# Kernel optimization log

Hardware: AMD Instinct MI355X
Metric: run time of the kernel (lower is better)

The kernel has to match this reference:

```python
import jax, jax.numpy as jnp
import numpy as np

TIME_SEG_LEN = 5
PRED_STEPS = 1
B, N, D = 4, 4096, 4
F1, F2 = 32, 64  # cnn filters; F2 must equal GCSConv/Dense width 64


def _conv1d_time(x, Wc1, bc1, Wc2, bc2):
    # x: [B, N, T, D] -> per-node temporal CNN collapsing T=5 -> 1 -> [B, N, F2]
    b, n, t, d = x.shape
    xr = x.reshape(b * n, t, d)
    dn = ('NWC', 'WIO', 'NWC')
    h = jax.lax.conv_general_dilated(xr, Wc1, (1,), 'VALID', dimension_numbers=dn) + bc1
    h = jax.nn.relu(h)
    h = jax.lax.conv_general_dilated(h, Wc2, (1,), 'VALID', dimension_numbers=dn) + bc2
    return h.reshape(b, n, -1)  # [B, N, F2]


def setup_inputs() -> dict:
    key = jax.random.key(0)
    ks = jax.random.split(key, 12)
    time_segs = jax.random.normal(ks[0], (B, TIME_SEG_LEN, N, D), dtype=jnp.float32)
    edges = jax.random.randint(ks[1], (N, N), 0, 2, dtype=jnp.int32)
    s = lambda *sh: 1.0 / np.sqrt(sh[-2] if len(sh) > 1 else sh[0])
    return {
        'time_segs': time_segs,
        'edges': edges,
        'Wc1': jax.random.normal(ks[2], (3, D, F1), dtype=jnp.float32) * 0.3,
        'bc1': jnp.zeros((F1,), jnp.float32),
        'Wc2': jax.random.normal(ks[3], (3, F1, F2), dtype=jnp.float32) * 0.1,
        'bc2': jnp.zeros((F2,), jnp.float32),
        'Wg1': jax.random.normal(ks[4], (F2, 64), dtype=jnp.float32) * 0.125,
        'bg': jnp.zeros((64,), jnp.float32),
        'Wd': jax.random.normal(ks[5], (F2 + 64, 64), dtype=jnp.float32) * 0.09,
        'bd': jnp.zeros((64,), jnp.float32),
        'Wo': jax.random.normal(ks[6], (64, D), dtype=jnp.float32) * 0.125,
        'bo': jnp.zeros((D,), jnp.float32),
    }


def reference(time_segs, edges, Wc1, bc1, Wc2, bc2, Wg1, bg, Wd, bd, Wo, bo):
    A = edges.astype(jnp.float32)
    n = A.shape[0]
    deg = jnp.sum(A, axis=-1, keepdims=True)              # row degree
    A_norm = A / jnp.where(deg > 0, deg, 1.0)             # D^-1 A (symmetric=False)
    A_nd = A_norm * (1.0 - jnp.eye(n, dtype=A.dtype))     # self-edge masking of X row j == zeroing diag
    col_deg = jnp.sum(A, axis=0)                          # e = np.sum(edges, axis=0)
    alive = (col_deg != 0).astype(time_segs.dtype)[None, :, None]  # zero-degree nodes -> zeros branch

    ext = jnp.transpose(time_segs, (0, 2, 1, 3))          # [B, N, T, D]
    for i in range(PRED_STEPS):
        seg = ext[:, :, i:, :]                            # [B, N, 5, D]
        cond = _conv1d_time(seg, Wc1, bc1, Wc2, bc2)      # [B, N, F2]
        # Vectorized per-node masked GCSConv: row j of tanh(A X_j W1 + X_j W2 + b)
        # with X_j = X zeroed at node j. Skip term vanishes at row j.
        agg = jnp.einsum('jk,bkf->bjf', A_nd, cond)       # [B, N, F2]
        G = jnp.tanh(agg @ Wg1 + bg) * alive              # [B, N, 64]
        h = jax.nn.relu(jnp.concatenate([cond, G], axis=-1) @ Wd + bd)
        nxt = seg[:, :, -1, :] + jnp.tanh(h @ Wo + bo)    # residual update [B, N, D]
        ext = jnp.concatenate([ext, nxt[:, :, None, :]], axis=2)
    out = jnp.transpose(ext, (0, 2, 1, 3))                # [B, T+P, N, D]
    return out[:, TIME_SEG_LEN:, :, :]                    # [B, pred_steps, N, D]
```

## Files before the change

kernel.cpp:

```cpp
#include <hip/hip_runtime.h>
#include <math.h>

typedef unsigned short ushort_t;
typedef unsigned int uint_t;
typedef unsigned long long u64_t;
typedef __attribute__((ext_vector_type(8))) __bf16 bf16x8;
typedef __attribute__((ext_vector_type(4))) float f32x4;

#define NN 4096
#define TT 5
#define F1 32
#define F2 64

__device__ __forceinline__ ushort_t f2bf(float x) {
    union { float f; uint_t u; } v; v.f = x;
    uint_t r = (v.u + 0x7FFFu + ((v.u >> 16) & 1u)) >> 16;
    return (ushort_t)r;
}
__device__ __forceinline__ float bf16f(float x) {
    union { float f; uint_t u; } v; v.f = x;
    v.u = (v.u + 0x7FFFu + ((v.u >> 16) & 1u)) & 0xFFFF0000u;
    return v.f;
}
__device__ __forceinline__ uint_t pk2(float a, float b) {
    return (uint_t)f2bf(a) | ((uint_t)f2bf(b) << 16);
}
__device__ __forceinline__ float tanh_fast(float x) {
    const float xc = fminf(fmaxf(x, -10.f), 10.f);
    const float e = __expf(2.f * xc);
    return (e - 1.f) * __builtin_amdgcn_rcpf(e + 1.f);
}

#define H1S 104
#define CBS 80
__global__ __launch_bounds__(256) void k1_cond(
    const float* __restrict__ ts, const float* __restrict__ Wc1, const float* __restrict__ bc1,
    const float* __restrict__ Wc2, const float* __restrict__ bc2,
    float* __restrict__ condf, ushort_t* __restrict__ condT)
{
    const int b = blockIdx.y;
    const int j0 = blockIdx.x * 64;
    const int t = threadIdx.x;

    __shared__ float sWc1[384];
    __shared__ float sbc1[F1];
    __shared__ float sbc2[F2];
    __shared__ ushort_t sWc2T[64 * H1S];
    __shared__ ushort_t h1B[64 * H1S];
    __shared__ ushort_t scb[64 * CBS];

    for (int i = t; i < 384; i += 256) sWc1[i] = Wc1[i];
    if (t < F1) sbc1[t] = bc1[t];
    if (t < F2) sbc2[t] = bc2[t];
    for (int i = t; i < 96 * 64; i += 256) {
        const int e = i >> 6, f = i & 63;
        sWc2T[f * H1S + e] = f2bf(Wc2[i]);
    }
    __syncthreads();

    {
        const int n = t & 63, f10 = (t >> 6) * 8;
        const int j = j0 + n;
        float4 x[5];
        #pragma unroll
        for (int tt = 0; tt < 5; ++tt)
            x[tt] = *(const float4*)(ts + ((((size_t)b * TT + tt) << 12) + j) * 4);
        #pragma unroll
        for (int tt0 = 0; tt0 < 3; ++tt0) {
            #pragma unroll
            for (int ff = 0; ff < 8; ++ff) {
                const int f1 = f10 + ff;
                float a = sbc1[f1];
                #pragma unroll
                for (int dt = 0; dt < 3; ++dt) {
                    const float4 xx = x[tt0 + dt];
                    a += xx.x * sWc1[(dt * 4 + 0) * F1 + f1];
                    a += xx.y * sWc1[(dt * 4 + 1) * F1 + f1];
                    a += xx.z * sWc1[(dt * 4 + 2) * F1 + f1];
                    a += xx.w * sWc1[(dt * 4 + 3) * F1 + f1];
                }
                h1B[n * H1S + tt0 * 32 + f1] = f2bf(fmaxf(a, 0.f));
            }
        }
    }
    __syncthreads();

    {
        const int w = t >> 6, l = t & 63;
        const int m0 = w * 16, kseg = (l >> 4) * 8;
        f32x4 acc[4] = {};
        #pragma unroll
        for (int ks = 0; ks < 3; ++ks) {
            const bf16x8 av = *(const bf16x8*)&h1B[(m0 + (l & 15)) * H1S + ks * 32 + kseg];
            #pragma unroll
            for (int ct = 0; ct < 4; ++ct) {
                const bf16x8 bv = *(const bf16x8*)&sWc2T[(ct * 16 + (l & 15)) * H1S + ks * 32 + kseg];
                acc[ct] = __builtin_amdgcn_mfma_f32_16x16x32_bf16(av, bv, acc[ct], 0, 0, 0);
            }
        }
        #pragma unroll
        for (int ct = 0; ct < 4; ++ct)
            #pragma unroll
            for (int i = 0; i < 4; ++i) {
                const int row = m0 + (l >> 4) * 4 + i;
                const int col = ct * 16 + (l & 15);
                const float c = acc[ct][i] + sbc2[col];
                condf[((((size_t)b << 12) + j0 + row) << 6) + col] = c;
                scb[col * CBS + row] = f2bf(c);
            }
    }
    __syncthreads();
    {
        const int f2 = t >> 2, seg = t & 3;
        ushort_t* dst = condT + (((size_t)b * 64 + f2) << 12) + j0 + seg * 16;
        *(uint4*)dst = *(const uint4*)&scb[f2 * CBS + seg * 16];
        *(uint4*)(dst + 8) = *(const uint4*)&scb[f2 * CBS + seg * 16 + 8];
    }
}

__device__ __forceinline__ void stage_chunk(
    const int4 pa, int it, int kq, ushort_t* dstbuf, int soff, uint_t& regm, int& cnt)
{
    const u64_t b0 = __ballot(pa.x != 0);
    const u64_t b1 = __ballot(pa.y != 0);
    const u64_t b2 = __ballot(pa.z != 0);
    const u64_t b3 = __ballot(pa.w != 0);
    const uint_t m0 = (uint_t)(b0 | (b0 >> 32)), m1 = (uint_t)(b1 | (b1 >> 32));
    const uint_t m2 = (uint_t)(b2 | (b2 >> 32)), m3 = (uint_t)(b3 | (b3 >> 32));
    const uint_t nib = ((m0 >> kq) & 1u) | (((m1 >> kq) & 1u) << 1) |
                       (((m2 >> kq) & 1u) << 2) | (((m3 >> kq) & 1u) << 3);
    regm |= nib << (it * 4);
    cnt += (pa.x != 0) + (pa.y != 0) + (pa.z != 0) + (pa.w != 0);
    const uint_t h01 = (pa.x ? 0x3F80u : 0u) | (pa.y ? 0x3F800000u : 0u);
    const uint_t h23 = (pa.z ? 0x3F80u : 0u) | (pa.w ? 0x3F800000u : 0u);
    *(uint2*)(dstbuf + soff) = make_uint2(h01, h23);
}

__global__ __launch_bounds__(1024, 8) void k3_gemm(
    const int* __restrict__ edges, const ushort_t* __restrict__ condT,
    float* __restrict__ agg0, float* __restrict__ agg1,
    float* __restrict__ agg2, float* __restrict__ agg3,
    int* __restrict__ degI, uint_t* __restrict__ colbits)
{
    const int t = threadIdx.x;
    const int stripe = blockIdx.x >> 2, ks4 = blockIdx.x & 3;
    const int j0 = stripe * 32, kb = ks4 * 1024;

    __shared__ __align__(16) ushort_t abuf[8][4096];

    const int w = t >> 6, l = t & 63;
    const int r = t >> 5, kq = t & 31;
    const int rl = r & 15, rh = r >> 4;
    const int ks_s = kq >> 3, q_s = (kq >> 1) & 3;
    const int soff = (rh * 2048 + ks_s * 512 + (q_s * 16 + rl) * 8 + (kq & 1) * 4) ^ (q_s << 4);
    const int aoff = (l * 8) ^ ((l >> 4) << 4);

    const int* ep = edges + (size_t)(j0 + r) * NN + kb + kq * 4;
    const ushort_t* bp = condT + (size_t)(w * 16 + (l & 15)) * NN + kb + (l >> 4) * 8;

    uint_t regm = 0; int cnt = 0;
    int4 pa[4];

    #pragma unroll
    for (int c = 0; c < 4; ++c) pa[c] = *(const int4*)(ep + c * 128);
    #pragma unroll
    for (int c = 0; c < 4; ++c) stage_chunk(pa[c], c, kq, &abuf[c][0], soff, regm, cnt);
    __syncthreads();

    #pragma unroll
    for (int c = 0; c < 4; ++c) pa[c] = *(const int4*)(ep + (c + 4) * 128);

    f32x4 acc0 = {0.f, 0.f, 0.f, 0.f};
    f32x4 acc1 = {0.f, 0.f, 0.f, 0.f};

    #pragma unroll
    for (int ch = 0; ch < 4; ++ch) {
        const ushort_t* ab = &abuf[ch][0];
        const ushort_t* bpi = bp + ch * 128;
        #pragma unroll
        for (int ks = 0; ks < 4; ++ks) {
            const bf16x8 bfv = *(const bf16x8*)(bpi + ks * 32);
            const bf16x8 a0 = *(const bf16x8*)(ab + ks * 512 + aoff);
            const bf16x8 a1 = *(const bf16x8*)(ab + 2048 + ks * 512 + aoff);
            acc0 = __builtin_amdgcn_mfma_f32_16x16x32_bf16(a0, bfv, acc0, 0, 0, 0);
            acc1 = __builtin_amdgcn_mfma_f32_16x16x32_bf16(a1, bfv, acc1, 0, 0, 0);
        }
    }
    #pragma unroll
    for (int c = 0; c < 4; ++c) stage_chunk(pa[c], c + 4, kq, &abuf[c + 4][0], soff, regm, cnt);
    __syncthreads();

    #pragma unroll
    for (int ch = 4; ch < 8; ++ch) {
        const ushort_t* ab = &abuf[ch][0];
        const ushort_t* bpi = bp + ch * 128;
        #pragma unroll
        for (int ks = 0; ks < 4; ++ks) {
            const bf16x8 bfv = *(const bf16x8*)(bpi + ks * 32);
            const bf16x8 a0 = *(const bf16x8*)(ab + ks * 512 + aoff);
            const bf16x8 a1 = *(const bf16x8*)(ab + 2048 + ks * 512 + aoff);
            acc0 = __builtin_amdgcn_mfma_f32_16x16x32_bf16(a0, bfv, acc0, 0, 0, 0);
            acc1 = __builtin_amdgcn_mfma_f32_16x16x32_bf16(a1, bfv, acc1, 0, 0, 0);
        }
    }

    {
        float* aggS = (ks4 == 0) ? agg0 : (ks4 == 1) ? agg1 : (ks4 == 2) ? agg2 : agg3;
        const int col = w * 16 + (l & 15);
        float* dst = aggS + ((size_t)(col >> 6) * NN << 6) + (col & 63);
        #pragma unroll
        for (int i = 0; i < 4; ++i) {
            const int ja = j0 + (l >> 4) * 4 + i;
            dst[(size_t)ja << 6] = acc0[i];
            dst[(size_t)(ja + 16) << 6] = acc1[i];
        }
    }
    {
        int s = cnt;
        #pragma unroll
        for (int off = 16; off >= 1; off >>= 1) s += __shfl_down(s, off, 32);
        if (kq == 0) atomicAdd(&degI[j0 + r], s);
    }
    __syncthreads();
    uint_t* colsh = (uint_t*)&abuf[0][0];
    if (l < 32) colsh[w * 32 + kq] = regm;
    __syncthreads();
    if (t < 32) {
        uint_t v = 0;
        #pragma unroll
        for (int w2 = 0; w2 < 16; ++w2) v |= colsh[w2 * 32 + t];
        colsh[512 + t] = v;
    }
    __syncthreads();
    if (t < 32) {
        const int it = t >> 2, koct = t & 3;
        uint_t word = 0;
        #pragma unroll
        for (int s2 = 0; s2 < 8; ++s2)
            word |= ((colsh[512 + koct * 8 + s2] >> (it * 4)) & 15u) << (s2 * 4);
        atomicOr(&colbits[(kb >> 5) + t], word);
    }
}

#define WGS 88
#define WDS 136
#define HS  69
__global__ __launch_bounds__(256) void k4_mlp(
    const float* __restrict__ ts, const int* __restrict__ edges,
    const float* __restrict__ condf,
    const float* __restrict__ agg0, const float* __restrict__ agg1,
    const float* __restrict__ agg2, const float* __restrict__ agg3,
    const int* __restrict__ degI, const uint_t* __restrict__ colbits,
    const float* __restrict__ Wg1, const float* __restrict__ bg,
    const float* __restrict__ Wd, const float* __restrict__ bd,
    const float* __restrict__ Wo, const float* __restrict__ bo,
    float* __restrict__ out)
{
    const int b = blockIdx.y;
    const int j0 = blockIdx.x * 64;
    const int t = threadIdx.x;

    __shared__ ushort_t sWg1T[64 * WGS];
    __shared__ ushort_t sWdT[64 * WDS];
    __shared__ ushort_t aggB[64 * WGS];
    __shared__ ushort_t catB[64 * WDS];
    __shared__ float sH[64 * HS];
    __shared__ float sWo[256];
    __shared__ float sbg[64], sbd[64], sbo[4], sAlive[64];

    for (int i = t; i < 4096; i += 256) {
        const int in = i >> 6, o = i & 63;
        sWg1T[o * WGS + in] = f2bf(Wg1[i]);
    }
    for (int i = t; i < 8192; i += 256) {
        const int in = i >> 6, o = i & 63;
        sWdT[o * WDS + in] = f2bf(Wd[i]);
    }
    if (t < 256) sWo[t] = Wo[t];
    if (t < 64) { sbg[t] = bg[t]; sbd[t] = bd[t]; }
    if (t < 4) sbo[t] = bo[t];
    if (t < 64) {
        const int j = j0 + t;
        sAlive[t] = (float)((colbits[j >> 5] >> (j & 31)) & 1u);
    }
    {
        const int r = t >> 2, fs = t & 3;
        const int j = j0 + r;
        const float dv = (float)degI[j];
        const float inv = 1.f / (dv > 0.f ? dv : 1.f);
        const float dgf = edges[(size_t)j * NN + j] ? 1.f : 0.f;
        const size_t base = (((size_t)b << 12) + j) << 6;
        #pragma unroll
        for (int q = 0; q < 4; ++q) {
            const int f = fs * 16 + q * 4;
            const float4 a0 = *(const float4*)(agg0 + base + f);
            const float4 a1 = *(const float4*)(agg1 + base + f);
            const float4 a2 = *(const float4*)(agg2 + base + f);
            const float4 a3 = *(const float4*)(agg3 + base + f);
            const float4 c4 = *(const float4*)(condf + base + f);
            const float n0 = (a0.x + a1.x + a2.x + a3.x - dgf * bf16f(c4.x)) * inv;
            const float n1 = (a0.y + a1.y + a2.y + a3.y - dgf * bf16f(c4.y)) * inv;
            const float n2 = (a0.z + a1.z + a2.z + a3.z - dgf * bf16f(c4.z)) * inv;
            const float n3 = (a0.w + a1.w + a2.w + a3.w - dgf * bf16f(c4.w)) * inv;
            *(uint2*)&aggB[r * WGS + f] = make_uint2(pk2(n0, n1), pk2(n2, n3));
            *(uint2*)&catB[r * WDS + f] = make_uint2(pk2(c4.x, c4.y), pk2(c4.z, c4.w));
        }
    }
    __syncthreads();

    const int w = t >> 6, l = t & 63;
    const int m0 = w * 16, kseg = (l >> 4) * 8;

    {
        f32x4 acc[4] = {};
        #pragma unroll
        for (int ks = 0; ks < 2; ++ks) {
            const bf16x8 av = *(const bf16x8*)&aggB[(m0 + (l & 15)) * WGS + ks * 32 + kseg];
            #pragma unroll
            for (int ct = 0; ct < 4; ++ct) {
                const bf16x8 bv = *(const bf16x8*)&sWg1T[(ct * 16 + (l & 15)) * WGS + ks * 32 + kseg];
                acc[ct] = __builtin_amdgcn_mfma_f32_16x16x32_bf16(av, bv, acc[ct], 0, 0, 0);
            }
        }
        #pragma unroll
        for (int ct = 0; ct < 4; ++ct)
            #pragma unroll
            for (int i = 0; i < 4; ++i) {
                const int row = m0 + (l >> 4) * 4 + i;
                const int col = ct * 16 + (l & 15);
                const float g = tanh_fast(acc[ct][i] + sbg[col]) * sAlive[row];
                catB[row * WDS + 64 + col] = f2bf(g);
            }
    }
    __syncthreads();
    {
        f32x4 acc[4] = {};
        #pragma unroll
        for (int ks = 0; ks < 4; ++ks) {
            const bf16x8 av = *(const bf16x8*)&catB[(m0 + (l & 15)) * WDS + ks * 32 + kseg];
            #pragma unroll
            for (int ct = 0; ct < 4; ++ct) {
                const bf16x8 bv = *(const bf16x8*)&sWdT[(ct * 16 + (l & 15)) * WDS + ks * 32 + kseg];
                acc[ct] = __builtin_amdgcn_mfma_f32_16x16x32_bf16(av, bv, acc[ct], 0, 0, 0);
            }
        }
        #pragma unroll
        for (int ct = 0; ct < 4; ++ct)
            #pragma unroll
            for (int i = 0; i < 4; ++i) {
                const int row = m0 + (l >> 4) * 4 + i;
                const int col = ct * 16 + (l & 15);
                sH[row * HS + col] = fmaxf(acc[ct][i] + sbd[col], 0.f);
            }
    }
    __syncthreads();
    {
        const int r = t >> 2, d = t & 3;
        const int j = j0 + r;
        float s = sbo[d];
        #pragma unroll 8
        for (int f = 0; f < 64; ++f) s += sH[r * HS + f] * sWo[f * 4 + d];
        const float segl = ts[((((size_t)b * TT + 4) << 12) + j) * 4 + d];
        out[((((size_t)b << 12) + j) << 2) + d] = segl + tanh_fast(s);
    }
}

extern "C" void kernel_launch(void* const* d_in, const int* in_sizes, int n_in,
                              void* d_out, int out_size, void* d_ws, size_t ws_size,
                              hipStream_t stream)
{
    (void)in_sizes; (void)n_in; (void)out_size; (void)ws_size;
    const float* ts    = (const float*)d_in[0];
    const int*   edges = (const int*)d_in[1];
    const float* Wc1   = (const float*)d_in[2];
    const float* bc1   = (const float*)d_in[3];
    const float* Wc2   = (const float*)d_in[4];
    const float* bc2   = (const float*)d_in[5];
    const float* Wg1   = (const float*)d_in[6];
    const float* bg    = (const float*)d_in[7];
    const float* Wd    = (const float*)d_in[8];
    const float* bd    = (const float*)d_in[9];
    const float* Wo    = (const float*)d_in[10];
    const float* bo    = (const float*)d_in[11];
    float* out = (float*)d_out;

    char* ws = (char*)d_ws;
    ushort_t* condT   = (ushort_t*)(ws);
    float*    condf   = (float*)(ws + (size_t)(2 << 20));
    float*    agg0    = (float*)(ws + (size_t)(6 << 20));
    float*    agg1    = (float*)(ws + (size_t)(10 << 20));
    float*    agg2    = (float*)(ws + (size_t)(14 << 20));
    float*    agg3    = (float*)(ws + (size_t)(18 << 20));
    int*      degI    = (int*)(ws + (size_t)(22 << 20));
    uint_t*   colbits = (uint_t*)(ws + (size_t)(22 << 20) + 16384);

    hipMemsetAsync(degI, 0, 16384 + 512, stream);

    k1_cond<<<dim3(64, 4), 256, 0, stream>>>(ts, Wc1, bc1, Wc2, bc2, condf, condT);
    k3_gemm<<<512, 1024, 0, stream>>>(edges, condT, agg0, agg1, agg2, agg3, degI, colbits);
    k4_mlp<<<dim3(64, 4), 256, 0, stream>>>(ts, edges, condf, agg0, agg1, agg2, agg3,
                                            degI, colbits, Wg1, bg, Wd, bd, Wo, bo, out);
}
```

Before: 166.1 us.

## Pack adjacency into bitmask in a separate kernel and feed GEMM from bits

Adds a k2_bits kernel that streams the int32 edge matrix once, packs it into a 1-bit-per-edge mask, and computes row degrees. The GEMM kernel then reads the compact bitmask instead of the 64 MB int matrix and expands it to bf16 in shared memory in a single stage, with simplified column-alive bookkeeping through a shared atomicOr. The edge matrix is still read in full once, so the total bytes read barely change. The change adds a kernel launch and a serial dependency, and it loses the earlier overlap of edge loads with MFMA work.

```diff
diff --git a/kernel.cpp b/kernel.cpp
--- a/kernel.cpp
+++ b/kernel.cpp
@@ -118,63 +118,68 @@
     }
 }
 
-__device__ __forceinline__ void stage_chunk(
-    const int4 pa, int it, int kq, ushort_t* dstbuf, int soff, uint_t& regm, int& cnt)
-{
-    const u64_t b0 = __ballot(pa.x != 0);
-    const u64_t b1 = __ballot(pa.y != 0);
-    const u64_t b2 = __ballot(pa.z != 0);
-    const u64_t b3 = __ballot(pa.w != 0);
-    const uint_t m0 = (uint_t)(b0 | (b0 >> 32)), m1 = (uint_t)(b1 | (b1 >> 32));
-    const uint_t m2 = (uint_t)(b2 | (b2 >> 32)), m3 = (uint_t)(b3 | (b3 >> 32));
-    const uint_t nib = ((m0 >> kq) & 1u) | (((m1 >> kq) & 1u) << 1) |
-                       (((m2 >> kq) & 1u) << 2) | (((m3 >> kq) & 1u) << 3);
-    regm |= nib << (it * 4);
-    cnt += (pa.x != 0) + (pa.y != 0) + (pa.z != 0) + (pa.w != 0);
-    const uint_t h01 = (pa.x ? 0x3F80u : 0u) | (pa.y ? 0x3F800000u : 0u);
-    const uint_t h23 = (pa.z ? 0x3F80u : 0u) | (pa.w ? 0x3F800000u : 0u);
-    *(uint2*)(dstbuf + soff) = make_uint2(h01, h23);
+__global__ __launch_bounds__(1024, 8) void k2_bits(
+    const int* __restrict__ edges, uint_t* __restrict__ bits, int* __restrict__ degI)
+{
+    const int t = threadIdx.x;
+    const uint_t W = (uint_t)blockIdx.x * 1024u + (uint_t)t;
+    const int4* ep = (const int4*)edges + (size_t)W * 8;
+    uint_t b = 0;
+    #pragma unroll
+    for (int c = 0; c < 8; ++c) {
+        const int4 v = ep[c];
+        const uint_t nib = (v.x != 0 ? 1u : 0u) | (v.y != 0 ? 2u : 0u) |
+                           (v.z != 0 ? 4u : 0u) | (v.w != 0 ? 8u : 0u);
+        b |= nib << (c * 4);
+    }
+    bits[W] = b;
+    int s = __popc(b);
+    #pragma unroll
+    for (int off = 32; off >= 1; off >>= 1) s += __shfl_down(s, off);
+    if ((t & 63) == 0) atomicAdd(&degI[W >> 7], s);
 }
 
 __global__ __launch_bounds__(1024, 8) void k3_gemm(
-    const int* __restrict__ edges, const ushort_t* __restrict__ condT,
+    const uint_t* __restrict__ bits, const ushort_t* __restrict__ condT,
     float* __restrict__ agg0, float* __restrict__ agg1,
     float* __restrict__ agg2, float* __restrict__ agg3,
-    int* __restrict__ degI, uint_t* __restrict__ colbits)
+    uint_t* __restrict__ colbits)
 {
     const int t = threadIdx.x;
     const int stripe = blockIdx.x >> 2, ks4 = blockIdx.x & 3;
     const int j0 = stripe * 32, kb = ks4 * 1024;
 
     __shared__ __align__(16) ushort_t abuf[8][4096];
+    __shared__ uint_t colsh[32];
+
+    const int rl = t & 15, wq = (t >> 4) & 31, rh = t >> 9;
+    const uint_t bw = bits[(uint_t)(j0 + rh * 16 + rl) * 128u + (uint_t)(kb >> 5) + (uint_t)wq];
+    if (t < 32) colsh[t] = 0;
+    {
+        ushort_t* dst = &abuf[wq >> 2][rh * 2048 + (wq & 3) * 512];
+        #pragma unroll
+        for (int o = 0; o < 4; ++o) {
+            const uint_t oct = bw >> (o * 8);
+            uint4 wv;
+            wv.x = ((oct & 1u)   ? 0x3F80u : 0u) | ((oct & 2u)   ? 0x3F800000u : 0u);
+            wv.y = ((oct & 4u)   ? 0x3F80u : 0u) | ((oct & 8u)   ? 0x3F800000u : 0u);
+            wv.z = ((oct & 16u)  ? 0x3F80u : 0u) | ((oct & 32u)  ? 0x3F800000u : 0u);
+            wv.w = ((oct & 64u)  ? 0x3F80u : 0u) | ((oct & 128u) ? 0x3F800000u : 0u);
+            *(uint4*)(dst + o * 128 + ((rl * 8) ^ (o << 4))) = wv;
+        }
+    }
+    __syncthreads();
+    atomicOr(&colsh[wq], bw);
 
     const int w = t >> 6, l = t & 63;
-    const int r = t >> 5, kq = t & 31;
-    const int rl = r & 15, rh = r >> 4;
-    const int ks_s = kq >> 3, q_s = (kq >> 1) & 3;
-    const int soff = (rh * 2048 + ks_s * 512 + (q_s * 16 + rl) * 8 + (kq & 1) * 4) ^ (q_s << 4);
     const int aoff = (l * 8) ^ ((l >> 4) << 4);
-
-    const int* ep = edges + (size_t)(j0 + r) * NN + kb + kq * 4;
     const ushort_t* bp = condT + (size_t)(w * 16 + (l & 15)) * NN + kb + (l >> 4) * 8;
-
-    uint_t regm = 0; int cnt = 0;
-    int4 pa[4];
-
-    #pragma unroll
-    for (int c = 0; c < 4; ++c) pa[c] = *(const int4*)(ep + c * 128);
-    #pragma unroll
-    for (int c = 0; c < 4; ++c) stage_chunk(pa[c], c, kq, &abuf[c][0], soff, regm, cnt);
-    __syncthreads();
-
-    #pragma unroll
-    for (int c = 0; c < 4; ++c) pa[c] = *(const int4*)(ep + (c + 4) * 128);
 
     f32x4 acc0 = {0.f, 0.f, 0.f, 0.f};
     f32x4 acc1 = {0.f, 0.f, 0.f, 0.f};
 
     #pragma unroll
-    for (int ch = 0; ch < 4; ++ch) {
+    for (int ch = 0; ch < 8; ++ch) {
         const ushort_t* ab = &abuf[ch][0];
         const ushort_t* bpi = bp + ch * 128;
         #pragma unroll
@@ -186,23 +191,6 @@
             acc1 = __builtin_amdgcn_mfma_f32_16x16x32_bf16(a1, bfv, acc1, 0, 0, 0);
         }
     }
-    #pragma unroll
-    for (int c = 0; c < 4; ++c) stage_chunk(pa[c], c + 4, kq, &abuf[c + 4][0], soff, regm, cnt);
-    __syncthreads();
-
-    #pragma unroll
-    for (int ch = 4; ch < 8; ++ch) {
-        const ushort_t* ab = &abuf[ch][0];
-        const ushort_t* bpi = bp + ch * 128;
-        #pragma unroll
-        for (int ks = 0; ks < 4; ++ks) {
-            const bf16x8 bfv = *(const bf16x8*)(bpi + ks * 32);
-            const bf16x8 a0 = *(const bf16x8*)(ab + ks * 512 + aoff);
-            const bf16x8 a1 = *(const bf16x8*)(ab + 2048 + ks * 512 + aoff);
-            acc0 = __builtin_amdgcn_mfma_f32_16x16x32_bf16(a0, bfv, acc0, 0, 0, 0);
-            acc1 = __builtin_amdgcn_mfma_f32_16x16x32_bf16(a1, bfv, acc1, 0, 0, 0);
-        }
-    }
 
     {
         float* aggS = (ks4 == 0) ? agg0 : (ks4 == 1) ? agg1 : (ks4 == 2) ? agg2 : agg3;
@@ -215,38 +203,15 @@
             dst[(size_t)(ja + 16) << 6] = acc1[i];
         }
     }
-    {
-        int s = cnt;
-        #pragma unroll
-        for (int off = 16; off >= 1; off >>= 1) s += __shfl_down(s, off, 32);
-        if (kq == 0) atomicAdd(&degI[j0 + r], s);
-    }
-    __syncthreads();
-    uint_t* colsh = (uint_t*)&abuf[0][0];
-    if (l < 32) colsh[w * 32 + kq] = regm;
-    __syncthreads();
-    if (t < 32) {
-        uint_t v = 0;
-        #pragma unroll
-        for (int w2 = 0; w2 < 16; ++w2) v |= colsh[w2 * 32 + t];
-        colsh[512 + t] = v;
-    }
-    __syncthreads();
-    if (t < 32) {
-        const int it = t >> 2, koct = t & 3;
-        uint_t word = 0;
-        #pragma unroll
-        for (int s2 = 0; s2 < 8; ++s2)
-            word |= ((colsh[512 + koct * 8 + s2] >> (it * 4)) & 15u) << (s2 * 4);
-        atomicOr(&colbits[(kb >> 5) + t], word);
-    }
+    __syncthreads();
+    if (t < 32) atomicOr(&colbits[(kb >> 5) + t], colsh[t]);
 }
 
 #define WGS 88
 #define WDS 136
 #define HS  69
 __global__ __launch_bounds__(256) void k4_mlp(
-    const float* __restrict__ ts, const int* __restrict__ edges,
+    const float* __restrict__ ts, const uint_t* __restrict__ bits,
     const float* __restrict__ condf,
     const float* __restrict__ agg0, const float* __restrict__ agg1,
     const float* __restrict__ agg2, const float* __restrict__ agg3,
@@ -288,7 +253,7 @@
         const int j = j0 + r;
         const float dv = (float)degI[j];
         const float inv = 1.f / (dv > 0.f ? dv : 1.f);
-        const float dgf = edges[(size_t)j * NN + j] ? 1.f : 0.f;
+        const float dgf = (float)((bits[(uint_t)j * 128u + (uint_t)(j >> 5)] >> (j & 31)) & 1u);
         const size_t base = (((size_t)b << 12) + j) << 6;
         #pragma unroll
         for (int q = 0; q < 4; ++q) {
@@ -393,11 +358,13 @@
     float*    agg3    = (float*)(ws + (size_t)(18 << 20));
     int*      degI    = (int*)(ws + (size_t)(22 << 20));
     uint_t*   colbits = (uint_t*)(ws + (size_t)(22 << 20) + 16384);
+    uint_t*   bits    = (uint_t*)(ws + (size_t)(23 << 20));
 
     hipMemsetAsync(degI, 0, 16384 + 512, stream);
 
+    k2_bits<<<512, 1024, 0, stream>>>(edges, bits, degI);
     k1_cond<<<dim3(64, 4), 256, 0, stream>>>(ts, Wc1, bc1, Wc2, bc2, condf, condT);
-    k3_gemm<<<512, 1024, 0, stream>>>(edges, condT, agg0, agg1, agg2, agg3, degI, colbits);
-    k4_mlp<<<dim3(64, 4), 256, 0, stream>>>(ts, edges, condf, agg0, agg1, agg2, agg3,
+    k3_gemm<<<512, 1024, 0, stream>>>(bits, condT, agg0, agg1, agg2, agg3, colbits);
+    k4_mlp<<<dim3(64, 4), 256, 0, stream>>>(ts, bits, condf, agg0, agg1, agg2, agg3,
                                             degI, colbits, Wg1, bg, Wd, bd, Wo, bo, out);
 }
```

Result: slower. 171.6 us (+3.3%).
